# Kernel tuning notes

Measured on AMD Instinct MI355X. Metric: run time of the kernel, lower is better.

The kernel has to match this reference:

```python
import jax, jax.numpy as jnp
import numpy as np

D_MODEL = 1024
N_HEADS = 16
HEAD_DIM = D_MODEL // N_HEADS


def setup_inputs() -> dict:
    key = jax.random.key(0)
    ks = jax.random.split(key, 5)
    B, S = 2, 2048
    x = jax.random.normal(ks[0], (B, S, D_MODEL), dtype=jnp.float32)
    # nn.Linear weights: [out_features, in_features]
    s_in = 1.0 / np.sqrt(D_MODEL)
    qkv_w = jax.random.uniform(ks[1], (3 * D_MODEL, D_MODEL), jnp.float32, -s_in, s_in)
    qkv_b = jax.random.uniform(ks[2], (3 * D_MODEL,), jnp.float32, -s_in, s_in)
    out_w = jax.random.uniform(ks[3], (D_MODEL, D_MODEL), jnp.float32, -s_in, s_in)
    out_b = jax.random.uniform(ks[4], (D_MODEL,), jnp.float32, -s_in, s_in)
    return {"x": x, "qkv_w": qkv_w, "qkv_b": qkv_b, "out_w": out_w, "out_b": out_b}


def reference(x, qkv_w, qkv_b, out_w, out_b):
    B, S, D = x.shape
    H, Hd = N_HEADS, HEAD_DIM
    scale = 1.0 / np.sqrt(Hd)
    qkv = jnp.einsum('bsd,ed->bse', x, qkv_w) + qkv_b  # [B,S,3D]
    qkv = qkv.reshape(B, S, 3, H, Hd)
    q = qkv[:, :, 0].transpose(0, 2, 1, 3)  # [B,H,S,Hd]
    k = qkv[:, :, 1].transpose(0, 2, 1, 3)
    v = qkv[:, :, 2].transpose(0, 2, 1, 3)
    scores = jnp.einsum('bhqd,bhkd->bhqk', q, k) * scale  # [B,H,S,S]
    causal = jnp.triu(jnp.ones((S, S), dtype=bool), k=1)
    scores = jnp.where(causal[None, None], -jnp.inf, scores)
    probs = jax.nn.softmax(scores, axis=-1)
    out = jnp.einsum('bhqk,bhkd->bhqd', probs, v)  # [B,H,S,Hd]
    out = out.transpose(0, 2, 1, 3).reshape(B, S, D)
    out = jnp.einsum('bsd,ed->bse', out, out_w) + out_b
    return out
```

## Files before the change

kernel.cpp:

```cpp
#include <hip/hip_runtime.h>
#include <hip/hip_bf16.h>

#define SEQ    2048
#define DMODEL 1024
#define NHEAD  16
#define HDIM   64
#define BATCH  2
#define NTOK   (BATCH * SEQ)

#define N_X   (NTOK * DMODEL)
#define N_WQ  (3 * DMODEL * DMODEL)
#define N_BQ  (3 * DMODEL)
#define N_WO  (DMODEL * DMODEL)
#define N_BO  (DMODEL)
#define N_CANON (N_X + N_WQ + N_BQ + N_WO + N_BO)

#define NEG_SENT (-1.0e30f)
#define QSCALE 0.1803368801111f

typedef __attribute__((ext_vector_type(8))) short short8;
typedef __attribute__((ext_vector_type(4))) short short4v;
typedef __attribute__((ext_vector_type(4))) float f32x4;
typedef __attribute__((ext_vector_type(16))) float f32x16;

#define MFMA_BF16(A, B, C) __builtin_amdgcn_mfma_f32_16x16x32_bf16((A), (B), (C), 0, 0, 0)
#define MFMA32_BF16(A, B, C) __builtin_amdgcn_mfma_f32_32x32x16_bf16((A), (B), (C), 0, 0, 0)

static __device__ __forceinline__ short8 load8(const __hip_bfloat16* p) {
    return *(const short8*)p;
}

static __device__ __forceinline__ unsigned cvtpk_bf16(float lo, float hi) {
    unsigned r;
    asm("v_cvt_pk_bf16_f32 %0, %1, %2" : "=v"(r) : "v"(lo), "v"(hi));
    return r;
}

static __device__ __forceinline__ void async16(const void* g, void* l) {
    __builtin_amdgcn_global_load_lds(
        (const __attribute__((address_space(1))) unsigned int*)g,
        (__attribute__((address_space(3))) unsigned int*)l,
        16, 0, 0);
}

__global__ void detect_kernel(const unsigned short* __restrict__ w, int* flag) {
    int cnt = 0;
    for (int i = threadIdx.x; i < 512; i += 64) {
        const unsigned e = (w[i] >> 7) & 0xFF;
        if (e >= 125) cnt++;
    }
#pragma unroll
    for (int o = 32; o; o >>= 1) cnt += __shfl_down(cnt, o);
    if (threadIdx.x == 0) *flag = (cnt > 8) ? 1 : 0;
}

__global__ __launch_bounds__(256) void canon_kernel(
    const void* __restrict__ s0, const void* __restrict__ s1,
    const void* __restrict__ s2, const void* __restrict__ s3,
    const void* __restrict__ s4,
    __hip_bfloat16* __restrict__ dst, const int* __restrict__ flag)
{
    const int v = blockIdx.x * 256 + threadIdx.x;
    if (v >= N_CANON / 8) return;
    const int idx = v * 8;
    const void* src;
    int off;
    if (idx < N_X)                          { src = s0; off = idx; }
    else if (idx < N_X + N_WQ)              { src = s1; off = idx - N_X; }
    else if (idx < N_X + N_WQ + N_BQ)       { src = s2; off = idx - (N_X + N_WQ); }
    else if (idx < N_X + N_WQ + N_BQ + N_WO){ src = s3; off = idx - (N_X + N_WQ + N_BQ); }
    else                                    { src = s4; off = idx - (N_X + N_WQ + N_BQ + N_WO); }
    if (*flag != 0) {
        const f32x4* sp = (const f32x4*)((const float*)src + off);
        const f32x4 x0 = sp[0], x1 = sp[1];
        short8 o;
#pragma unroll
        for (int j = 0; j < 4; ++j) {
            o[j]     = (short)__bfloat16_as_ushort(__float2bfloat16(x0[j]));
            o[4 + j] = (short)__bfloat16_as_ushort(__float2bfloat16(x1[j]));
        }
        *(short8*)&dst[idx] = o;
    } else {
        *(short8*)&dst[idx] = *(const short8*)((const __hip_bfloat16*)src + off);
    }
}

__global__ __launch_bounds__(256) void qkv_gemm_kernel(
    const __hip_bfloat16* __restrict__ X,
    const __hip_bfloat16* __restrict__ W,
    const __hip_bfloat16* __restrict__ bias,
    __hip_bfloat16* __restrict__ Qs,
    __hip_bfloat16* __restrict__ Kb,
    __hip_bfloat16* __restrict__ Vt)
{
    constexpr int Kd = DMODEL;
    __shared__ __align__(16) __hip_bfloat16 As[3][128 * 32];
    __shared__ __align__(16) __hip_bfloat16 Bs[3][128 * 32];

    const int tid   = threadIdx.x;
    const int lane  = tid & 63;
    const int w     = tid >> 6;
    const int mTile = blockIdx.y * 128;
    const int nTile = blockIdx.x * 128;
    const int wm    = (w >> 1) * 64;
    const int wn    = (w & 1) * 64;
    const int lm    = lane & 15;
    const int q4    = lane >> 4;
    const int lks   = (q4 ^ ((lm >> 1) & 3)) * 8;

    f32x4 acc[4][4];
#pragma unroll
    for (int i = 0; i < 4; ++i)
#pragma unroll
        for (int j = 0; j < 4; ++j)
            acc[i][j] = (f32x4){0.f, 0.f, 0.f, 0.f};

    const int r0c = tid >> 2;
    const int r1c = (tid + 256) >> 2;
    const int cbs = ((tid & 3) ^ ((tid >> 3) & 3)) * 8;

    const __hip_bfloat16* gA0 = &X[(size_t)(mTile + r0c) * Kd + cbs];
    const __hip_bfloat16* gA1 = &X[(size_t)(mTile + r1c) * Kd + cbs];
    const __hip_bfloat16* gB0 = &W[(size_t)(nTile + r0c) * Kd + cbs];
    const __hip_bfloat16* gB1 = &W[(size_t)(nTile + r1c) * Kd + cbs];

    async16(gA0, (char*)As[0] + tid * 16);
    async16(gA1, (char*)As[0] + tid * 16 + 4096);
    async16(gB0, (char*)Bs[0] + tid * 16);
    async16(gB1, (char*)Bs[0] + tid * 16 + 4096);
    async16(gA0 + 32, (char*)As[1] + tid * 16);
    async16(gA1 + 32, (char*)As[1] + tid * 16 + 4096);
    async16(gB0 + 32, (char*)Bs[1] + tid * 16);
    async16(gB1 + 32, (char*)Bs[1] + tid * 16 + 4096);

    int cur = 0;
    constexpr int NIT = Kd / 32;
    for (int it = 0; it < NIT; ++it) {
        if (it + 1 < NIT) {
            asm volatile("s_waitcnt vmcnt(4)" ::: "memory");
        } else {
            asm volatile("s_waitcnt vmcnt(0)" ::: "memory");
        }
        __builtin_amdgcn_s_barrier();
        __builtin_amdgcn_sched_barrier(0);

        if (it + 2 < NIT) {
            const int slot = (cur + 2 >= 3) ? cur - 1 : cur + 2;
            const int k2 = (it + 2) * 32;
            async16(gA0 + k2, (char*)As[slot] + tid * 16);
            async16(gA1 + k2, (char*)As[slot] + tid * 16 + 4096);
            async16(gB0 + k2, (char*)Bs[slot] + tid * 16);
            async16(gB1 + k2, (char*)Bs[slot] + tid * 16 + 4096);
        }

        const __hip_bfloat16* Ac = As[cur];
        const __hip_bfloat16* Bc = Bs[cur];
        short8 a[4], b[4];
#pragma unroll
        for (int i = 0; i < 4; ++i)
            a[i] = *(const short8*)&Ac[(wm + i * 16 + lm) * 32 + lks];
#pragma unroll
        for (int j = 0; j < 4; ++j)
            b[j] = *(const short8*)&Bc[(wn + j * 16 + lm) * 32 + lks];
#pragma unroll
        for (int i = 0; i < 4; ++i)
#pragma unroll
            for (int j = 0; j < 4; ++j)
                acc[i][j] = MFMA_BF16(a[i], b[j], acc[i][j]);

        cur = (cur + 1 == 3) ? 0 : cur + 1;
    }

    const int r0 = (lane >> 4) * 4;
#pragma unroll
    for (int j = 0; j < 4; ++j) {
        const int n  = nTile + wn + j * 16 + lm;
        const float bv = __bfloat162float(bias[n]);
        const int c = n >> 10;
        const int h = (n >> 6) & 15;
        const int d = n & 63;
#pragma unroll
        for (int i = 0; i < 4; ++i) {
            if (c == 2) {
                const int m0 = mTile + wm + i * 16 + r0;
                const int bb = m0 >> 11;
                const int s0 = m0 & (SEQ - 1);
                const int bh = bb * NHEAD + h;
                short4v pk;
#pragma unroll
                for (int r = 0; r < 4; ++r)
                    pk[r] = (short)__bfloat16_as_ushort(
                        __float2bfloat16(acc[i][j][r] + bv));
                *(short4v*)&Vt[(size_t)(bh * HDIM + d) * SEQ + s0] = pk;
            } else {
#pragma unroll
                for (int r = 0; r < 4; ++r) {
                    const int m  = mTile + wm + i * 16 + r0 + r;
                    const int bb = m >> 11;
                    const int s  = m & (SEQ - 1);
                    const int bh = bb * NHEAD + h;
                    const float v = acc[i][j][r] + bv;
                    if (c == 0) {
                        Qs[(size_t)(bh * SEQ + s) * HDIM + d] = __float2bfloat16(v * QSCALE);
                    } else {
                        Kb[(size_t)(bh * SEQ + s) * HDIM + d] = __float2bfloat16(v);
                    }
                }
            }
        }
    }
}

__global__ __launch_bounds__(256, 3) void attn_kernel(
    const __hip_bfloat16* __restrict__ Qs,
    const __hip_bfloat16* __restrict__ Kb,
    const __hip_bfloat16* __restrict__ Vt,
    float* __restrict__ Opart,
    float* __restrict__ MLpart)
{
    __shared__ __align__(16) __hip_bfloat16 Kt[2][64 * 64];
    __shared__ __align__(16) __hip_bfloat16 Vs[2][64 * 64];

    const int tid  = threadIdx.x;
    const int lane = tid & 63;
    const int wv   = tid >> 6;
    const int bh   = blockIdx.x;
    const int py   = blockIdx.y;
    const int p    = py / 3;
    const int j3   = py % 3;

    const int c_lo = (j3 == 0) ? 0 : (j3 == 1 ? 12 : 23);
    const int c_hi = (j3 == 0) ? 12 : (j3 == 1 ? 23 : 34);
    const int bnd  = 32 - 2 * p;

    const int lq = lane & 31;
    const int sg = lane >> 5;
    const int swr = lq & 7;

    const __hip_bfloat16* Qbh = Qs + (size_t)bh * SEQ * HDIM;
    const __hip_bfloat16* Kbh = Kb + (size_t)bh * SEQ * HDIM;
    const __hip_bfloat16* Vbh = Vt + (size_t)bh * HDIM * SEQ;

    const int srow0 = tid >> 3;
    const int scb   = (tid & 7) ^ (srow0 & 7);

    for (int seg = 0; seg < 2; ++seg) {
        int qb, a, b, slot;
        if (seg == 0) {
            if (j3 == 2 && p >= 5) continue;
            qb = 15 - p; a = c_lo;
            b  = (c_hi < bnd) ? c_hi : bnd;
            slot = j3;
        } else {
            if (j3 == 0 || (j3 == 1 && p <= 4)) continue;
            qb = p;
            a  = ((c_lo > bnd) ? c_lo : bnd) - bnd;
            b  = c_hi - bnd;
            slot = (j3 == 2) ? 3 : 4;
        }

        const int wbase = qb * 128 + wv * 32;
        const int qrow  = wbase + lq;

        short8 qa[4];
#pragma unroll
        for (int s = 0; s < 4; ++s)
            qa[s] = load8(&Qbh[(size_t)qrow * HDIM + s * 16 + sg * 8]);

        float m_run = NEG_SENT;
        float l_run = 0.f;
        f32x16 Oacc[2];
#pragma unroll
        for (int t = 0; t < 2; ++t)
#pragma unroll
            for (int e = 0; e < 16; ++e) Oacc[t][e] = 0.f;

        __builtin_amdgcn_s_barrier();

        {
            const int kk0 = a * 64;
            async16(&Kbh[(size_t)(kk0 + srow0) * HDIM + scb * 8],      (char*)Kt[0] + tid * 16);
            async16(&Kbh[(size_t)(kk0 + srow0 + 32) * HDIM + scb * 8], (char*)Kt[0] + tid * 16 + 4096);
            async16(&Vbh[(size_t)srow0 * SEQ + kk0 + scb * 8],         (char*)Vs[0] + tid * 16);
            async16(&Vbh[(size_t)(srow0 + 32) * SEQ + kk0 + scb * 8],  (char*)Vs[0] + tid * 16 + 4096);
            if (a + 1 < b) {
                const int kk1 = kk0 + 64;
                async16(&Kbh[(size_t)(kk1 + srow0) * HDIM + scb * 8],      (char*)Kt[1] + tid * 16);
                async16(&Kbh[(size_t)(kk1 + srow0 + 32) * HDIM + scb * 8], (char*)Kt[1] + tid * 16 + 4096);
                async16(&Vbh[(size_t)srow0 * SEQ + kk1 + scb * 8],         (char*)Vs[1] + tid * 16);
                async16(&Vbh[(size_t)(srow0 + 32) * SEQ + kk1 + scb * 8],  (char*)Vs[1] + tid * 16 + 4096);
            }
        }

        int cur = 0;
        for (int ci = a; ci < b; ++ci) {
            const int k0 = ci * 64;

            if (ci + 1 < b) {
                asm volatile("s_waitcnt vmcnt(4)" ::: "memory");
            } else {
                asm volatile("s_waitcnt vmcnt(0)" ::: "memory");
            }
            __builtin_amdgcn_s_barrier();
            __builtin_amdgcn_sched_barrier(0);

            if (k0 <= wbase + 31) {
                const __hip_bfloat16* Kc = Kt[cur];
                const __hip_bfloat16* Vc = Vs[cur];

                f32x16 sc[2];
#pragma unroll
                for (int t = 0; t < 2; ++t)
#pragma unroll
                    for (int e = 0; e < 16; ++e) sc[t][e] = 0.f;
#pragma unroll
                for (int t = 0; t < 2; ++t)
#pragma unroll
                    for (int s = 0; s < 4; ++s) {
                        const short8 ka = *(const short8*)&Kc[
                            (t * 32 + lq) * 64 + (((s * 2 + sg) ^ swr) * 8)];
                        sc[t] = MFMA32_BF16(ka, qa[s], sc[t]);
                    }

                if (k0 + 63 > wbase) {
#pragma unroll
                    for (int t = 0; t < 2; ++t)
#pragma unroll
                        for (int g = 0; g < 4; ++g)
#pragma unroll
                            for (int r = 0; r < 4; ++r) {
                                const int key = k0 + t * 32 + r + 8 * g + 4 * sg;
                                if (key > qrow) sc[t][g * 4 + r] = NEG_SENT;
                            }
                }

                float mx = sc[0][0];
#pragma unroll
                for (int t = 0; t < 2; ++t)
#pragma unroll
                    for (int e = 0; e < 16; ++e) mx = fmaxf(mx, sc[t][e]);
                mx = fmaxf(mx, __shfl_xor(mx, 32));

                if (!__all(mx <= m_run + 8.0f)) {
                    const float mn = fmaxf(m_run, mx);
                    const float alpha = exp2f(m_run - mn);
                    m_run = mn;
                    l_run *= alpha;
#pragma unroll
                    for (int t = 0; t < 2; ++t)
#pragma unroll
                        for (int e = 0; e < 16; ++e) Oacc[t][e] *= alpha;
                }

                float ssum = 0.f;
#pragma unroll
                for (int t = 0; t < 2; ++t)
#pragma unroll
                    for (int e = 0; e < 16; ++e) {
                        const float pv = exp2f(sc[t][e] - m_run);
                        sc[t][e] = pv;
                        ssum += pv;
                    }
                ssum += __shfl_xor(ssum, 32);
                l_run += ssum;

                unsigned wpk[2][4][2];
#pragma unroll
                for (int t = 0; t < 2; ++t)
#pragma unroll
                    for (int g = 0; g < 4; ++g) {
                        wpk[t][g][0] = cvtpk_bf16(sc[t][g * 4 + 0], sc[t][g * 4 + 1]);
                        wpk[t][g][1] = cvtpk_bf16(sc[t][g * 4 + 2], sc[t][g * 4 + 3]);
                    }

#pragma unroll
                for (int s = 0; s < 4; ++s) {
                    const int t  = s >> 1;
                    const int gp = (s & 1) * 2;
                    const unsigned oe0 = wpk[t][gp][0],     oe1 = wpk[t][gp][1];
                    const unsigned oo0 = wpk[t][gp + 1][0], oo1 = wpk[t][gp + 1][1];
                    const unsigned pay0 = sg ? oe0 : oo0;
                    const unsigned pay1 = sg ? oe1 : oo1;
                    const unsigned rc0 = (unsigned)__shfl_xor((int)pay0, 32);
                    const unsigned rc1 = (unsigned)__shfl_xor((int)pay1, 32);
                    unsigned f[4];
                    f[0] = sg ? rc0 : oe0;
                    f[1] = sg ? rc1 : oe1;
                    f[2] = sg ? oo0 : rc0;
                    f[3] = sg ? oo1 : rc1;
                    const short8 pa = *(const short8*)f;
#pragma unroll
                    for (int t2 = 0; t2 < 2; ++t2) {
                        const short8 va = *(const short8*)&Vc[
                            (t2 * 32 + lq) * 64 + (((s * 2 + sg) ^ swr) * 8)];
                        Oacc[t2] = MFMA32_BF16(va, pa, Oacc[t2]);
                    }
                }
            }

            __builtin_amdgcn_s_barrier();
            if (ci + 2 < b) {
                const int kk = (ci + 2) * 64;
                async16(&Kbh[(size_t)(kk + srow0) * HDIM + scb * 8],      (char*)Kt[cur] + tid * 16);
                async16(&Kbh[(size_t)(kk + srow0 + 32) * HDIM + scb * 8], (char*)Kt[cur] + tid * 16 + 4096);
                async16(&Vbh[(size_t)srow0 * SEQ + kk + scb * 8],         (char*)Vs[cur] + tid * 16);
                async16(&Vbh[(size_t)(srow0 + 32) * SEQ + kk + scb * 8],  (char*)Vs[cur] + tid * 16 + 4096);
            }
            cur ^= 1;
        }

        const size_t pbase = ((size_t)(bh * 8 + p) * 5 + slot) * 128;
        const size_t orow  = (pbase + wv * 32 + lq) * 64;
#pragma unroll
        for (int t2 = 0; t2 < 2; ++t2)
#pragma unroll
            for (int g = 0; g < 4; ++g) {
                f32x4 v;
#pragma unroll
                for (int r = 0; r < 4; ++r) v[r] = Oacc[t2][g * 4 + r];
                *(f32x4*)&Opart[orow + t2 * 32 + 8 * g + 4 * sg] = v;
            }
        if (lane < 32) {
            MLpart[(pbase + wv * 32 + lane) * 2 + 0] = m_run;
            MLpart[(pbase + wv * 32 + lane) * 2 + 1] = l_run;
        }
    }
}

__global__ __launch_bounds__(256) void attn_merge_kernel(
    const float* __restrict__ Opart, const float* __restrict__ MLpart,
    __hip_bfloat16* __restrict__ O)
{
    const int idx  = blockIdx.x * 256 + threadIdx.x;
    const int d16  = idx & 3;
    const int grow = idx >> 2;
    const int bh   = grow >> 11;
    const int s    = grow & 2047;
    const int qb   = s >> 7;
    const int rin  = s & 127;

    const bool heavy = (qb >= 8);
    const int p  = heavy ? (15 - qb) : qb;
    const int s0 = heavy ? 0 : 3;
    const int s1 = heavy ? 1 : 4;
    const bool v1 = heavy ? true : (p >= 5);
    const bool v2 = heavy && (p <= 4);

    const size_t rb = (size_t)(bh * 8 + p) * 5;
    const size_t r0 = (rb + s0) * 128 + rin;
    const size_t r1 = (rb + s1) * 128 + rin;
    const size_t r2 = (rb + 2)  * 128 + rin;

    const float m0 = MLpart[r0 * 2],                 l0 = MLpart[r0 * 2 + 1];
    const float m1 = v1 ? MLpart[r1 * 2] : NEG_SENT, l1 = v1 ? MLpart[r1 * 2 + 1] : 0.f;
    const float m2 = v2 ? MLpart[r2 * 2] : NEG_SENT, l2 = v2 ? MLpart[r2 * 2 + 1] : 0.f;

    float mm = fmaxf(m0, fmaxf(m1, m2));
    const float a0 = exp2f(m0 - mm);
    const float a1 = v1 ? exp2f(m1 - mm) : 0.f;
    const float a2 = v2 ? exp2f(m2 - mm) : 0.f;
    const float inv = 1.0f / (a0 * l0 + a1 * l1 + a2 * l2);

    f32x4 o[4];
    {
        const f32x4* O0 = (const f32x4*)&Opart[r0 * 64 + d16 * 16];
#pragma unroll
        for (int v = 0; v < 4; ++v) o[v] = a0 * O0[v];
    }
    if (v1) {
        const f32x4* O1 = (const f32x4*)&Opart[r1 * 64 + d16 * 16];
#pragma unroll
        for (int v = 0; v < 4; ++v) o[v] += a1 * O1[v];
    }
    if (v2) {
        const f32x4* O2 = (const f32x4*)&Opart[r2 * 64 + d16 * 16];
#pragma unroll
        for (int v = 0; v < 4; ++v) o[v] += a2 * O2[v];
    }

    short8 out[2];
#pragma unroll
    for (int v = 0; v < 4; ++v)
#pragma unroll
        for (int jj = 0; jj < 4; ++jj)
            out[v >> 1][(v & 1) * 4 + jj] = (short)__bfloat16_as_ushort(
                __float2bfloat16(o[v][jj] * inv));

    const int b = bh >> 4, hh = bh & 15;
    __hip_bfloat16* dst = &O[((size_t)b * SEQ + s) * DMODEL + hh * 64 + d16 * 16];
    ((short8*)dst)[0] = out[0];
    ((short8*)dst)[1] = out[1];
}

__global__ __launch_bounds__(256) void proj_gemm_kernel(
    const __hip_bfloat16* __restrict__ A,
    const __hip_bfloat16* __restrict__ W,
    const __hip_bfloat16* __restrict__ bias,
    void* __restrict__ outv,
    const int* __restrict__ flag)
{
    constexpr int Kd = DMODEL;
    __shared__ __align__(16) __hip_bfloat16 As[3][128 * 32];
    __shared__ __align__(16) __hip_bfloat16 Bs[3][64 * 32];

    const int tid   = threadIdx.x;
    const int lane  = tid & 63;
    const int w     = tid >> 6;
    const int mTile = blockIdx.y * 128;
    const int nTile = blockIdx.x * 64;
    const int wm    = (w >> 1) * 64;
    const int wn    = (w & 1) * 32;
    const int lm    = lane & 15;
    const int q4    = lane >> 4;
    const int lks   = (q4 ^ ((lm >> 1) & 3)) * 8;
    const bool f32out = (*flag != 0);

    f32x4 acc[4][2];
#pragma unroll
    for (int i = 0; i < 4; ++i)
#pragma unroll
        for (int j = 0; j < 2; ++j)
            acc[i][j] = (f32x4){0.f, 0.f, 0.f, 0.f};

    const int r0c = tid >> 2;
    const int r1c = (tid + 256) >> 2;
    const int cbs = ((tid & 3) ^ ((tid >> 3) & 3)) * 8;

    const __hip_bfloat16* gA0 = &A[(size_t)(mTile + r0c) * Kd + cbs];
    const __hip_bfloat16* gA1 = &A[(size_t)(mTile + r1c) * Kd + cbs];
    const __hip_bfloat16* gB0 = &W[(size_t)(nTile + r0c) * Kd + cbs];

    async16(gA0, (char*)As[0] + tid * 16);
    async16(gA1, (char*)As[0] + tid * 16 + 4096);
    async16(gB0, (char*)Bs[0] + tid * 16);
    async16(gA0 + 32, (char*)As[1] + tid * 16);
    async16(gA1 + 32, (char*)As[1] + tid * 16 + 4096);
    async16(gB0 + 32, (char*)Bs[1] + tid * 16);

    int cur = 0;
    constexpr int NIT = Kd / 32;
    for (int it = 0; it < NIT; ++it) {
        if (it + 1 < NIT) {
            asm volatile("s_waitcnt vmcnt(3)" ::: "memory");
        } else {
            asm volatile("s_waitcnt vmcnt(0)" ::: "memory");
        }
        __builtin_amdgcn_s_barrier();
        __builtin_amdgcn_sched_barrier(0);

        if (it + 2 < NIT) {
            const int slot = (cur + 2 >= 3) ? cur - 1 : cur + 2;
            const int k2 = (it + 2) * 32;
            async16(gA0 + k2, (char*)As[slot] + tid * 16);
            async16(gA1 + k2, (char*)As[slot] + tid * 16 + 4096);
            async16(gB0 + k2, (char*)Bs[slot] + tid * 16);
        }

        const __hip_bfloat16* Ac = As[cur];
        const __hip_bfloat16* Bc = Bs[cur];
        short8 a[4], b[2];
#pragma unroll
        for (int i = 0; i < 4; ++i)
            a[i] = *(const short8*)&Ac[(wm + i * 16 + lm) * 32 + lks];
#pragma unroll
        for (int j = 0; j < 2; ++j)
            b[j] = *(const short8*)&Bc[(wn + j * 16 + lm) * 32 + lks];
#pragma unroll
        for (int i = 0; i < 4; ++i)
#pragma unroll
            for (int j = 0; j < 2; ++j)
                acc[i][j] = MFMA_BF16(a[i], b[j], acc[i][j]);

        cur = (cur + 1 == 3) ? 0 : cur + 1;
    }

    const int r0 = (lane >> 4) * 4;
#pragma unroll
    for (int j = 0; j < 2; ++j) {
        const int n = nTile + wn + j * 16 + lm;
        const float bv = __bfloat162float(bias[n]);
#pragma unroll
        for (int i = 0; i < 4; ++i) {
#pragma unroll
            for (int r = 0; r < 4; ++r) {
                const size_t m = mTile + wm + i * 16 + r0 + r;
                const float v = acc[i][j][r] + bv;
                if (f32out) ((float*)outv)[m * DMODEL + n] = v;
                else ((__hip_bfloat16*)outv)[m * DMODEL + n] = __float2bfloat16(v);
            }
        }
    }
}

extern "C" void kernel_launch(void* const* d_in, const int* in_sizes, int n_in,
                              void* d_out, int out_size, void* d_ws, size_t ws_size,
                              hipStream_t stream) {
    const size_t OFF_CANON = 256;
    const size_t OFF_QS = OFF_CANON + (size_t)N_CANON * 2;
    const size_t OFF_KB = OFF_QS + (size_t)NTOK * DMODEL * 2;
    const size_t OFF_VT = OFF_KB + (size_t)NTOK * DMODEL * 2;
    const size_t OFF_AO = OFF_VT + (size_t)NTOK * DMODEL * 2;
    const size_t OFF_OP = OFF_AO + (size_t)NTOK * DMODEL * 2;
    const size_t OFF_ML = OFF_OP + (size_t)32 * 8 * 5 * 128 * 64 * 4;

    char* wsb = (char*)d_ws;
    int* flag = (int*)wsb;
    __hip_bfloat16* canon = (__hip_bfloat16*)(wsb + OFF_CANON);
    __hip_bfloat16* Xc = canon;
    __hip_bfloat16* Wq = Xc + N_X;
    __hip_bfloat16* Bq = Wq + N_WQ;
    __hip_bfloat16* Wo = Bq + N_BQ;
    __hip_bfloat16* Bo = Wo + N_WO;
    __hip_bfloat16* Qs = (__hip_bfloat16*)(wsb + OFF_QS);
    __hip_bfloat16* Kb = (__hip_bfloat16*)(wsb + OFF_KB);
    __hip_bfloat16* Vt = (__hip_bfloat16*)(wsb + OFF_VT);
    __hip_bfloat16* Ao = (__hip_bfloat16*)(wsb + OFF_AO);
    float* Opart = (float*)(wsb + OFF_OP);
    float* MLpart = (float*)(wsb + OFF_ML);

    detect_kernel<<<1, 64, 0, stream>>>((const unsigned short*)d_in[1], flag);
    canon_kernel<<<(N_CANON / 8 + 255) / 256, 256, 0, stream>>>(
        d_in[0], d_in[1], d_in[2], d_in[3], d_in[4], canon, flag);

    {
        dim3 grid(3 * DMODEL / 128, NTOK / 128);
        qkv_gemm_kernel<<<grid, 256, 0, stream>>>(Xc, Wq, Bq, Qs, Kb, Vt);
    }
    {
        dim3 grid(BATCH * NHEAD, 24);
        attn_kernel<<<grid, 256, 0, stream>>>(Qs, Kb, Vt, Opart, MLpart);
        attn_merge_kernel<<<(NTOK * NHEAD * 4) / 256, 256, 0, stream>>>(
            Opart, MLpart, Ao);
    }
    {
        dim3 grid(DMODEL / 64, NTOK / 128);
        proj_gemm_kernel<<<grid, 256, 0, stream>>>(Ao, Wo, Bo, d_out, flag);
    }
}
```

Measured before the change: 191.2 us.

## Fuse attention split-merge into attn kernel via last-arriver atomics; fold detect into canon

Removes the separate attention merge kernel. Each split block writes its partial O and m/l, then increments a per-tile atomic counter, and the last block to arrive merges the partials and writes the bf16 output directly. Blocks that alone own a query tile write the normalized output with no partials at all. The detect kernel is folded into every canon block, which recomputes the dtype flag locally, and a memset is added to clear the counters. This trades one kernel launch and some partial-buffer traffic for threadfence/atomic synchronisation and a merge tail on the last block.

```diff
diff --git a/kernel.cpp b/kernel.cpp
--- a/kernel.cpp
+++ b/kernel.cpp
@@ -43,23 +43,30 @@
         16, 0, 0);
 }
 
-__global__ void detect_kernel(const unsigned short* __restrict__ w, int* flag) {
-    int cnt = 0;
-    for (int i = threadIdx.x; i < 512; i += 64) {
-        const unsigned e = (w[i] >> 7) & 0xFF;
-        if (e >= 125) cnt++;
-    }
-#pragma unroll
-    for (int o = 32; o; o >>= 1) cnt += __shfl_down(cnt, o);
-    if (threadIdx.x == 0) *flag = (cnt > 8) ? 1 : 0;
-}
-
 __global__ __launch_bounds__(256) void canon_kernel(
     const void* __restrict__ s0, const void* __restrict__ s1,
     const void* __restrict__ s2, const void* __restrict__ s3,
     const void* __restrict__ s4,
-    __hip_bfloat16* __restrict__ dst, const int* __restrict__ flag)
+    __hip_bfloat16* __restrict__ dst, int* __restrict__ flag)
 {
+    __shared__ int sflag;
+    {
+        const unsigned short* w = (const unsigned short*)s1;
+        if (threadIdx.x < 64) {
+            int cnt = 0;
+            for (int i = threadIdx.x; i < 512; i += 64) {
+                const unsigned e = (w[i] >> 7) & 0xFF;
+                if (e >= 125) cnt++;
+            }
+#pragma unroll
+            for (int o = 32; o; o >>= 1) cnt += __shfl_down(cnt, o);
+            if (threadIdx.x == 0) sflag = (cnt > 8) ? 1 : 0;
+        }
+        __syncthreads();
+    }
+    const int isf32 = sflag;
+    if (blockIdx.x == 0 && threadIdx.x == 0) *flag = isf32;
+
     const int v = blockIdx.x * 256 + threadIdx.x;
     if (v >= N_CANON / 8) return;
     const int idx = v * 8;
@@ -70,7 +77,7 @@
     else if (idx < N_X + N_WQ + N_BQ)       { src = s2; off = idx - (N_X + N_WQ); }
     else if (idx < N_X + N_WQ + N_BQ + N_WO){ src = s3; off = idx - (N_X + N_WQ + N_BQ); }
     else                                    { src = s4; off = idx - (N_X + N_WQ + N_BQ + N_WO); }
-    if (*flag != 0) {
+    if (isf32) {
         const f32x4* sp = (const f32x4*)((const float*)src + off);
         const f32x4 x0 = sp[0], x1 = sp[1];
         short8 o;
@@ -216,10 +223,13 @@
     const __hip_bfloat16* __restrict__ Kb,
     const __hip_bfloat16* __restrict__ Vt,
     float* __restrict__ Opart,
-    float* __restrict__ MLpart)
+    float* __restrict__ MLpart,
+    __hip_bfloat16* __restrict__ O,
+    int* __restrict__ cnt)
 {
     __shared__ __align__(16) __hip_bfloat16 Kt[2][64 * 64];
     __shared__ __align__(16) __hip_bfloat16 Vs[2][64 * 64];
+    __shared__ int lastf;
 
     const int tid  = threadIdx.x;
     const int lane = tid & 63;
@@ -409,87 +419,95 @@
             cur ^= 1;
         }
 
-        const size_t pbase = ((size_t)(bh * 8 + p) * 5 + slot) * 128;
-        const size_t orow  = (pbase + wv * 32 + lq) * 64;
-#pragma unroll
-        for (int t2 = 0; t2 < 2; ++t2)
-#pragma unroll
-            for (int g = 0; g < 4; ++g) {
-                f32x4 v;
-#pragma unroll
-                for (int r = 0; r < 4; ++r) v[r] = Oacc[t2][g * 4 + r];
-                *(f32x4*)&Opart[orow + t2 * 32 + 8 * g + 4 * sg] = v;
-            }
-        if (lane < 32) {
-            MLpart[(pbase + wv * 32 + lane) * 2 + 0] = m_run;
-            MLpart[(pbase + wv * 32 + lane) * 2 + 1] = l_run;
-        }
-    }
-}
-
-__global__ __launch_bounds__(256) void attn_merge_kernel(
-    const float* __restrict__ Opart, const float* __restrict__ MLpart,
-    __hip_bfloat16* __restrict__ O)
-{
-    const int idx  = blockIdx.x * 256 + threadIdx.x;
-    const int d16  = idx & 3;
-    const int grow = idx >> 2;
-    const int bh   = grow >> 11;
-    const int s    = grow & 2047;
-    const int qb   = s >> 7;
-    const int rin  = s & 127;
-
-    const bool heavy = (qb >= 8);
-    const int p  = heavy ? (15 - qb) : qb;
-    const int s0 = heavy ? 0 : 3;
-    const int s1 = heavy ? 1 : 4;
-    const bool v1 = heavy ? true : (p >= 5);
-    const bool v2 = heavy && (p <= 4);
-
-    const size_t rb = (size_t)(bh * 8 + p) * 5;
-    const size_t r0 = (rb + s0) * 128 + rin;
-    const size_t r1 = (rb + s1) * 128 + rin;
-    const size_t r2 = (rb + 2)  * 128 + rin;
-
-    const float m0 = MLpart[r0 * 2],                 l0 = MLpart[r0 * 2 + 1];
-    const float m1 = v1 ? MLpart[r1 * 2] : NEG_SENT, l1 = v1 ? MLpart[r1 * 2 + 1] : 0.f;
-    const float m2 = v2 ? MLpart[r2 * 2] : NEG_SENT, l2 = v2 ? MLpart[r2 * 2 + 1] : 0.f;
-
-    float mm = fmaxf(m0, fmaxf(m1, m2));
-    const float a0 = exp2f(m0 - mm);
-    const float a1 = v1 ? exp2f(m1 - mm) : 0.f;
-    const float a2 = v2 ? exp2f(m2 - mm) : 0.f;
-    const float inv = 1.0f / (a0 * l0 + a1 * l1 + a2 * l2);
-
-    f32x4 o[4];
-    {
-        const f32x4* O0 = (const f32x4*)&Opart[r0 * 64 + d16 * 16];
-#pragma unroll
-        for (int v = 0; v < 4; ++v) o[v] = a0 * O0[v];
-    }
-    if (v1) {
-        const f32x4* O1 = (const f32x4*)&Opart[r1 * 64 + d16 * 16];
-#pragma unroll
-        for (int v = 0; v < 4; ++v) o[v] += a1 * O1[v];
-    }
-    if (v2) {
-        const f32x4* O2 = (const f32x4*)&Opart[r2 * 64 + d16 * 16];
-#pragma unroll
-        for (int v = 0; v < 4; ++v) o[v] += a2 * O2[v];
-    }
-
-    short8 out[2];
-#pragma unroll
-    for (int v = 0; v < 4; ++v)
-#pragma unroll
-        for (int jj = 0; jj < 4; ++jj)
-            out[v >> 1][(v & 1) * 4 + jj] = (short)__bfloat16_as_ushort(
-                __float2bfloat16(o[v][jj] * inv));
-
-    const int b = bh >> 4, hh = bh & 15;
-    __hip_bfloat16* dst = &O[((size_t)b * SEQ + s) * DMODEL + hh * 64 + d16 * 16];
-    ((short8*)dst)[0] = out[0];
-    ((short8*)dst)[1] = out[1];
+        const int b_  = bh >> 4, hh = bh & 15;
+        const int row = wv * 32 + lq;
+        const int sG  = qb * 128 + row;
+
+        if (seg == 1 && p <= 4) {
+            const float inv = 1.0f / l_run;
+            __hip_bfloat16* dst = &O[((size_t)b_ * SEQ + sG) * DMODEL + hh * 64];
+#pragma unroll
+            for (int t2 = 0; t2 < 2; ++t2)
+#pragma unroll
+                for (int g = 0; g < 4; ++g) {
+                    short4v pk;
+#pragma unroll
+                    for (int r = 0; r < 4; ++r)
+                        pk[r] = (short)__bfloat16_as_ushort(
+                            __float2bfloat16(Oacc[t2][g * 4 + r] * inv));
+                    *(short4v*)&dst[t2 * 32 + 8 * g + 4 * sg] = pk;
+                }
+        } else {
+            const size_t rb    = (size_t)(bh * 8 + p) * 5;
+            const size_t pbase = (rb + slot) * 128;
+#pragma unroll
+            for (int t2 = 0; t2 < 2; ++t2)
+#pragma unroll
+                for (int g = 0; g < 4; ++g) {
+                    f32x4 v;
+#pragma unroll
+                    for (int r = 0; r < 4; ++r) v[r] = Oacc[t2][g * 4 + r];
+                    *(f32x4*)&Opart[(pbase + row) * 64 + t2 * 32 + 8 * g + 4 * sg] = v;
+                }
+            if (lane < 32) {
+                MLpart[(pbase + wv * 32 + lane) * 2 + 0] = m_run;
+                MLpart[(pbase + wv * 32 + lane) * 2 + 1] = l_run;
+            }
+            __threadfence();
+            __syncthreads();
+            const int expc = (seg == 0) ? ((p <= 4) ? 3 : 2) : 2;
+            if (tid == 0) {
+                const int old = atomicAdd(&cnt[(bh * 8 + p) * 2 + seg], 1);
+                lastf = (old == expc - 1) ? 1 : 0;
+            }
+            __syncthreads();
+            if (lastf) {
+                __threadfence();
+                int os0, os1;
+                if (seg == 0) {
+                    if (p <= 4) { os0 = (slot + 1) % 3; os1 = (slot + 2) % 3; }
+                    else        { os0 = 1 - slot;       os1 = -1; }
+                } else          { os0 = 7 - slot;       os1 = -1; }
+
+                const float mo0 = MLpart[((rb + os0) * 128 + row) * 2 + 0];
+                const float lo0 = MLpart[((rb + os0) * 128 + row) * 2 + 1];
+                float mo1 = NEG_SENT, lo1 = 0.f;
+                if (os1 >= 0) {
+                    mo1 = MLpart[((rb + os1) * 128 + row) * 2 + 0];
+                    lo1 = MLpart[((rb + os1) * 128 + row) * 2 + 1];
+                }
+                const float mf = fmaxf(m_run, fmaxf(mo0, mo1));
+                const float aS = exp2f(m_run - mf);
+                const float a0 = exp2f(mo0 - mf);
+                const float a1 = (os1 >= 0) ? exp2f(mo1 - mf) : 0.f;
+                const float inv = 1.0f / (aS * l_run + a0 * lo0 + a1 * lo1);
+
+                __hip_bfloat16* dst = &O[((size_t)b_ * SEQ + sG) * DMODEL + hh * 64];
+#pragma unroll
+                for (int t2 = 0; t2 < 2; ++t2)
+#pragma unroll
+                    for (int g = 0; g < 4; ++g) {
+                        const int d0 = t2 * 32 + 8 * g + 4 * sg;
+                        const f32x4 v0 = *(const f32x4*)&Opart[((rb + os0) * 128 + row) * 64 + d0];
+                        f32x4 ac;
+#pragma unroll
+                        for (int r = 0; r < 4; ++r)
+                            ac[r] = aS * Oacc[t2][g * 4 + r] + a0 * v0[r];
+                        if (os1 >= 0) {
+                            const f32x4 v1 = *(const f32x4*)&Opart[((rb + os1) * 128 + row) * 64 + d0];
+#pragma unroll
+                            for (int r = 0; r < 4; ++r) ac[r] += a1 * v1[r];
+                        }
+                        short4v pk;
+#pragma unroll
+                        for (int r = 0; r < 4; ++r)
+                            pk[r] = (short)__bfloat16_as_ushort(
+                                __float2bfloat16(ac[r] * inv));
+                        *(short4v*)&dst[d0] = pk;
+                    }
+            }
+        }
+    }
 }
 
 __global__ __launch_bounds__(256) void proj_gemm_kernel(
@@ -602,6 +620,7 @@
     const size_t OFF_AO = OFF_VT + (size_t)NTOK * DMODEL * 2;
     const size_t OFF_OP = OFF_AO + (size_t)NTOK * DMODEL * 2;
     const size_t OFF_ML = OFF_OP + (size_t)32 * 8 * 5 * 128 * 64 * 4;
+    const size_t OFF_CNT = OFF_ML + (size_t)32 * 8 * 5 * 128 * 2 * 4;
 
     char* wsb = (char*)d_ws;
     int* flag = (int*)wsb;
@@ -617,8 +636,10 @@
     __hip_bfloat16* Ao = (__hip_bfloat16*)(wsb + OFF_AO);
     float* Opart = (float*)(wsb + OFF_OP);
     float* MLpart = (float*)(wsb + OFF_ML);
-
-    detect_kernel<<<1, 64, 0, stream>>>((const unsigned short*)d_in[1], flag);
+    int* cnt = (int*)(wsb + OFF_CNT);
+
+    hipMemsetAsync(cnt, 0, 32 * 8 * 2 * sizeof(int), stream);
+
     canon_kernel<<<(N_CANON / 8 + 255) / 256, 256, 0, stream>>>(
         d_in[0], d_in[1], d_in[2], d_in[3], d_in[4], canon, flag);
 
@@ -628,9 +649,7 @@
     }
     {
         dim3 grid(BATCH * NHEAD, 24);
-        attn_kernel<<<grid, 256, 0, stream>>>(Qs, Kb, Vt, Opart, MLpart);
-        attn_merge_kernel<<<(NTOK * NHEAD * 4) / 256, 256, 0, stream>>>(
-            Opart, MLpart, Ao);
+        attn_kernel<<<grid, 256, 0, stream>>>(Qs, Kb, Vt, Opart, MLpart, Ao, cnt);
     }
     {
         dim3 grid(DMODEL / 64, NTOK / 128);
```

After: 351.8 us. 84.0% more time.
